# Performance work log

Measured on AMD Instinct MI355X. Metric: run time of the kernel, lower is better.

## Reference

```python
import jax, jax.numpy as jnp
import numpy as np

B, T, L, IN, D, H = 2, 16, 256, 768, 1024, 16
HD = D // H
NREG = 4
P = NREG + 2          # frozen prefix: registers + noise + action
DEPTH = 8
TINT = 4              # temporal_attention_interval
CTX = 30              # temporal_context_length
BASE = 1000.0         # rope_base
EPS = 1e-6            # qk_norm_eps / rmsnorm eps
HID = 4096            # 4.0 * latent_dim
S = L + P             # tokens per frame


def _rms(x, w=None, eps=EPS):
    y = x * jax.lax.rsqrt(jnp.mean(x * x, axis=-1, keepdims=True) + eps)
    return y * w if w is not None else y


def _rope_cache(n, hd, base):
    inv = base ** (-jnp.arange(0, hd, 2, dtype=jnp.float32) / hd)
    ang = jnp.arange(n, dtype=jnp.float32)[:, None] * inv[None, :]  # [n, hd/2]
    return jnp.cos(ang), jnp.sin(ang)


def _apply_rope(x, cos, sin):
    x1, x2 = x[..., ::2], x[..., 1::2]
    return jnp.stack([x1 * cos - x2 * sin, x1 * sin + x2 * cos], axis=-1).reshape(x.shape)


def _attn(x, Wqkv, Wo, cos, sin, mask):
    # x: [..., S, D]; mask: bool, True = attend, broadcastable to [..., H, S, S]
    qkv = x @ Wqkv
    q, k, v = jnp.split(qkv, 3, axis=-1)
    heads = lambda t: t.reshape(t.shape[:-1] + (H, HD)).swapaxes(-2, -3)  # [..., H, S, HD]
    q, k, v = heads(q), heads(k), heads(v)
    q = _apply_rope(_rms(q), cos, sin)   # qk-norm then RoPE
    k = _apply_rope(_rms(k), cos, sin)
    s = jnp.einsum('...qd,...kd->...qk', q, k) / jnp.sqrt(jnp.float32(HD))
    s = jnp.where(mask, s, jnp.float32(-1e9))
    p = jax.nn.softmax(s, axis=-1) * mask.any(axis=-1, keepdims=True)  # zero rows with no allowed keys
    o = jnp.einsum('...qk,...kd->...qd', p, v)
    return o.swapaxes(-2, -3).reshape(x.shape) @ Wo


def _spatial_mask():
    m = np.zeros((S, S), bool)
    r, n, a, ls = NREG, NREG, NREG + 1, NREG + 2
    m[ls:, ls:] = True; m[ls:, n] = True; m[ls:, a] = True; m[ls:, :r] = True
    m[n, n] = True; m[a, a] = True
    m[:r, ls:] = True; m[:r, n] = True; m[:r, a] = True; m[:r, :r] = True
    return jnp.asarray(m)


def _temporal_mask(indep):
    m = jnp.tril(jnp.ones((T, T), bool), -1)  # strictly-past causal
    if CTX is not None and CTX < T:
        m = m & jnp.triu(m, -CTX)             # sliding context window
    m = jnp.broadcast_to(m, (B, T, T))
    m = jnp.where(indep[:, None, None], False, m)
    return m[:, None, None]  # [B,1,1,T,T] -> broadcasts over token pos and heads


def setup_inputs() -> dict:
    key = jax.random.key(0)
    ks = iter(jax.random.split(key, 40))
    g = lambda shape, s=0.02: jax.random.normal(next(ks), shape, jnp.float32) * s
    inp = {
        'noisy_latents': jax.random.normal(next(ks), (B, T, L, IN), jnp.float32),
        'noise_levels': jax.random.uniform(next(ks), (B, T), jnp.float32),
        'actions': jax.random.normal(next(ks), (B, T, 6), jnp.float32),
        'independent_frames_mask': jnp.zeros((B,), bool),
        'actions_mask': jnp.ones((B, T), bool),
        'W_in': g((IN, D)),
        'noise_w1': g((1, D)), 'noise_b1': jnp.zeros((D,), jnp.float32),
        'noise_w2': g((D, D)), 'noise_b2': jnp.zeros((D,), jnp.float32),
        'base_action_embed': g((D,)),
        'action_w': g((6, D)), 'action_b': jnp.zeros((D,), jnp.float32),
        'registers': g((NREG, D)),
        'ln1_w': jnp.ones((DEPTH, D), jnp.float32),
        'Wqkv_s': g((DEPTH, D, 3 * D)), 'Wo_s': g((DEPTH, D, D)),
        'lnt_w': jnp.ones((DEPTH, D), jnp.float32),
        'Wqkv_t': g((DEPTH, D, 3 * D)), 'Wo_t': g((DEPTH, D, D)),
        'ln2_w': jnp.ones((DEPTH, D), jnp.float32),
        'W1': g((DEPTH, D, HID)), 'W2': g((DEPTH, D, HID)), 'W3': g((DEPTH, HID, D)),
        'final_w': jnp.ones((D,), jnp.float32),
        'W_out': g((D, IN)), 'b_out': jnp.zeros((IN,), jnp.float32),
    }
    return inp


def reference(noisy_latents, noise_levels, actions, independent_frames_mask, actions_mask,
              W_in, noise_w1, noise_b1, noise_w2, noise_b2, base_action_embed,
              action_w, action_b, registers, ln1_w, Wqkv_s, Wo_s, lnt_w, Wqkv_t, Wo_t,
              ln2_w, W1, W2, W3, final_w, W_out, b_out):
    noisy_tokens = noisy_latents @ W_in                                   # [B,T,L,D]
    base = jnp.broadcast_to(base_action_embed, (B, T, 1, D))
    act = base + (actions @ action_w + action_b)[:, :, None, :]
    act = jnp.where(actions_mask[:, :, None, None], act, base)            # [B,T,1,D]
    nz = jax.nn.silu(noise_levels[..., None] @ noise_w1 + noise_b1) @ noise_w2 + noise_b2
    nz = nz[:, :, None, :]                                                # [B,T,1,D]
    reg = jnp.broadcast_to(registers, (B, T, NREG, D))
    x = jnp.concatenate([reg, nz, act, noisy_tokens], axis=2)             # [B,T,S,D]

    sp_mask = _spatial_mask()
    tm_mask = _temporal_mask(independent_frames_mask)
    sp_cos, sp_sin = _rope_cache(S, HD, BASE)
    tm_cos, tm_sin = _rope_cache(T, HD, BASE)
    keep_tok = (jnp.arange(S) >= P)[None, :, None, None]                  # zero temporal update on frozen prefix

    for i in range(DEPTH):
        h = _rms(x, ln1_w[i])
        x = x + _attn(h, Wqkv_s[i], Wo_s[i], sp_cos, sp_sin, sp_mask)
        if i % TINT == 0:
            ht = _rms(x, lnt_w[i]).transpose(0, 2, 1, 3)                  # [B,S,T,D]
            ot = _attn(ht, Wqkv_t[i], Wo_t[i], tm_cos, tm_sin, tm_mask)
            x = x + (ot * keep_tok).transpose(0, 2, 1, 3)
        h2 = _rms(x, ln2_w[i])
        x = x + (jax.nn.silu(h2 @ W1[i]) * (h2 @ W2[i])) @ W3[i]

    latents = _rms(x[..., P:, :], final_w)
    pred_clean_latents = latents @ W_out + b_out                          # [B,T,L,IN]
    return pred_clean_latents
```

## Files before the change

kernel.cpp:

```cpp
#include <hip/hip_runtime.h>
#include <cstdint>
#include <cstddef>

#define DEV __device__ __forceinline__

typedef __attribute__((ext_vector_type(8))) __bf16 bf16x8;
typedef __attribute__((ext_vector_type(4))) float f32x4;

#define NTOK   8384
#define NTOKP  8448
#define NLAT   8192

DEV float b2f(unsigned short u) {
  unsigned int x = ((unsigned int)u) << 16;
  return __builtin_bit_cast(float, x);
}
DEV unsigned short f2b(float f) {
  unsigned int x = __builtin_bit_cast(unsigned int, f);
  x += 0x7fffu + ((x >> 16) & 1u);
  return (unsigned short)(x >> 16);
}
DEV float wred_sum(float v) {
#pragma unroll
  for (int o = 32; o; o >>= 1) v += __shfl_xor(v, o);
  return v;
}
DEV bool mask_or(const void* p, int i) {
  return ((const unsigned char*)p)[i] != 0 || ((const int*)p)[i] != 0;
}
DEV bool mask_and(const void* p, int i) {
  return ((const unsigned char*)p)[i] != 0 && ((const int*)p)[i] != 0;
}
DEV void wgb() {
  asm volatile("" ::: "memory");
  __builtin_amdgcn_s_barrier();
  asm volatile("" ::: "memory");
}


__global__ void conv_f2b(const float* __restrict__ in, unsigned short* __restrict__ out, int n4) {
  int i = blockIdx.x * 256 + threadIdx.x;
  if (i < n4) {
    float4 v = ((const float4*)in)[i];
    ushort4 o;
    o.x = f2b(v.x); o.y = f2b(v.y); o.z = f2b(v.z); o.w = f2b(v.w);
    ((ushort4*)out)[i] = o;
  }
}

__global__ void build_rope(float2* __restrict__ out, int npos) {
  int idx = blockIdx.x * 256 + threadIdx.x;
  if (idx >= npos * 32) return;
  int pos = idx >> 5, i = idx & 31;
  float inv = powf(1000.0f, -(float)(2 * i) * (1.0f / 64.0f));
  float ang = (float)pos * inv;
  float sv, cv;
  sincosf(ang, &sv, &cv);
  out[idx] = make_float2(cv, sv);
}

__global__ __launch_bounds__(256) void transpose_w(const float* __restrict__ in,
                                                   unsigned short* __restrict__ out,
                                                   int K, int N, int ostride) {
  __shared__ float tile[32][33];
  int kb = blockIdx.x * 32, nb = blockIdx.y * 32;
  int tx = threadIdx.x & 31, ty = threadIdx.x >> 5;
#pragma unroll
  for (int i = 0; i < 32; i += 8)
    tile[ty + i][tx] = in[(size_t)(kb + ty + i) * N + (nb + tx)];
  __syncthreads();
#pragma unroll
  for (int i = 0; i < 32; i += 8)
    out[(size_t)(nb + ty + i) * ostride + (kb + tx)] = f2b(tile[tx][ty + i]);
}

__global__ __launch_bounds__(256) void noise_h1(const float* __restrict__ nlvl,
                                                const float* __restrict__ w1,
                                                const float* __restrict__ b1,
                                                const float* __restrict__ b2,
                                                float* __restrict__ h1,
                                                float* __restrict__ nz) {
  int i = blockIdx.x * 256 + threadIdx.x;
  int bt = i >> 10, d = i & 1023;
  float v = nlvl[bt] * w1[d] + b1[d];
  h1[i] = v / (1.0f + expf(-v));
  nz[i] = b2[d];
}

__global__ __launch_bounds__(256) void noise_mm(const float* __restrict__ h1,
                                                const float* __restrict__ w2,
                                                float* __restrict__ nz) {
  __shared__ float hs[32][128];
  int kc = blockIdx.x >> 4, dpg = blockIdx.x & 15;
  int tid = threadIdx.x;
  int k0 = kc * 128;
  for (int idx = tid; idx < 32 * 128; idx += 256) {
    int bt = idx >> 7, k = idx & 127;
    hs[bt][k] = h1[bt * 1024 + k0 + k];
  }
  __syncthreads();
  int dp = dpg * 64 + (tid & 63);
  int bt0 = (tid >> 6) * 8;
  float acc[8] = {};
  for (int k = 0; k < 128; ++k) {
    float w = w2[(size_t)(k0 + k) * 1024 + dp];
#pragma unroll
    for (int j = 0; j < 8; ++j) acc[j] += hs[bt0 + j][k] * w;
  }
#pragma unroll
  for (int j = 0; j < 8; ++j) atomicAdd(&nz[(bt0 + j) * 1024 + dp], acc[j]);
}

__global__ void embed_special(float* __restrict__ x, const float* __restrict__ regs,
                              const float* __restrict__ nz, const float* __restrict__ base_emb,
                              const float* __restrict__ actions, const float* __restrict__ action_w,
                              const float* __restrict__ action_b,
                              const void* __restrict__ amask) {
  int bt = blockIdx.x, d = threadIdx.x;
  float* xr = x + (size_t)bt * 262 * 1024;
#pragma unroll
  for (int r = 0; r < 4; ++r) xr[r * 1024 + d] = regs[r * 1024 + d];
  xr[4 * 1024 + d] = nz[(size_t)bt * 1024 + d];
  float a = base_emb[d];
  if (mask_or(amask, bt)) {
    float s = action_b[d];
#pragma unroll
    for (int i = 0; i < 6; ++i) s += actions[bt * 6 + i] * action_w[i * 1024 + d];
    a += s;
  }
  xr[5 * 1024 + d] = a;
}

template <bool REMAP>
__global__ __launch_bounds__(256) void rms_k(const float* __restrict__ x,
                                             const float* __restrict__ w,
                                             unsigned short* __restrict__ out) {
  int m = blockIdx.x, tid = threadIdx.x;
  size_t src = REMAP ? ((size_t)(m >> 8) * 262 + 6 + (m & 255)) : (size_t)m;
  float4 v = ((const float4*)(x + src * 1024))[tid];
  float ss = v.x * v.x + v.y * v.y + v.z * v.z + v.w * v.w;
  ss = wred_sum(ss);
  __shared__ float sred[4];
  if ((tid & 63) == 0) sred[tid >> 6] = ss;
  __syncthreads();
  float tot = sred[0] + sred[1] + sred[2] + sred[3];
  float sc = rsqrtf(tot * (1.0f / 1024.0f) + 1e-6f);
  float4 wv = ((const float4*)w)[tid];
  ushort4 o;
  o.x = f2b(v.x * sc * wv.x); o.y = f2b(v.y * sc * wv.y);
  o.z = f2b(v.z * sc * wv.z); o.w = f2b(v.w * sc * wv.w);
  ((ushort4*)(out + (size_t)m * 1024))[tid] = o;
}

#define KSTR 72
#define VSTR 296
__global__ __launch_bounds__(256) void attn_spatial(const unsigned short* __restrict__ qkv,
                                                    unsigned short* __restrict__ o,
                                                    const float2* __restrict__ rope) {
  __shared__ unsigned short Ks[272 * KSTR];
  __shared__ unsigned short Vt[64 * VSTR];
  __shared__ unsigned short Ps[4][16 * VSTR];
  const int h = blockIdx.x & 15;
  const int bt = blockIdx.x >> 4;
  const int tid = threadIdx.x, wave = tid >> 6, lane = tid & 63;
  const size_t tb = (size_t)bt * 262;

  {
    const int d = lane;
#pragma unroll 1
    for (int pss = 0; pss < 17; ++pss) {
      const int t0 = (pss * 4 + wave) * 4;
      ushort4 vp;
      unsigned short* vpp = (unsigned short*)&vp;
#pragma unroll
      for (int j = 0; j < 4; ++j) {
        const int t = t0 + j;
        float kv = 0.f, vv = 0.f;
        if (t < 262) {
          const size_t rb = (tb + t) * 3072 + h * 64 + d;
          kv = b2f(qkv[rb + 1024]);
          vv = b2f(qkv[rb + 2048]);
        }
        float ss = wred_sum(kv * kv);
        kv *= rsqrtf(ss * (1.0f / 64.0f) + 1e-6f);
        float partner = __shfl_xor(kv, 1);
        const int tc = t < 262 ? t : 261;
        float2 cs = rope[tc * 32 + (d >> 1)];
        kv = ((d & 1) == 0) ? (kv * cs.x - partner * cs.y)
                            : (partner * cs.y + kv * cs.x);
        Ks[t * KSTR + d] = f2b(kv);
        vpp[j] = f2b(vv);
      }
      *(ushort4*)(&Vt[d * VSTR + t0]) = vp;
    }
    for (int idx = tid; idx < 64 * 24; idx += 256) {
      Vt[(idx / 24) * VSTR + 272 + (idx % 24)] = 0;
    }
    for (int idx = tid; idx < 4 * 16 * 34; idx += 256) {
      int w = idx / (16 * 34), r = (idx / 34) & 15, c = idx % 34;
      Ps[w][r * VSTR + 262 + c] = 0;
    }
  }
  __syncthreads();

  unsigned short* Pw = &Ps[wave][0];
  const int kcol = lane & 15;
  const int g8 = (lane >> 4) << 3;
  const int g4 = g8 >> 1;
  const int rq = (lane >> 4) << 2;

#pragma unroll 1
  for (int qc = wave; qc < 17; qc += 4) {
    const int q0 = qc * 16;
    const int qrow = q0 + kcol;
    const int grow = qrow < 262 ? qrow : 261;
    const unsigned short* qp = qkv + (tb + grow) * 3072 + h * 64 + g8;
    float qv[16];
    {
      ushort4 a = *(const ushort4*)qp, b = *(const ushort4*)(qp + 4);
      ushort4 c = *(const ushort4*)(qp + 32), e = *(const ushort4*)(qp + 36);
      qv[0] = b2f(a.x); qv[1] = b2f(a.y); qv[2] = b2f(a.z); qv[3] = b2f(a.w);
      qv[4] = b2f(b.x); qv[5] = b2f(b.y); qv[6] = b2f(b.z); qv[7] = b2f(b.w);
      qv[8] = b2f(c.x); qv[9] = b2f(c.y); qv[10] = b2f(c.z); qv[11] = b2f(c.w);
      qv[12] = b2f(e.x); qv[13] = b2f(e.y); qv[14] = b2f(e.z); qv[15] = b2f(e.w);
    }
    float ss = 0.f;
#pragma unroll
    for (int i = 0; i < 16; ++i) ss += qv[i] * qv[i];
    ss += __shfl_xor(ss, 16);
    ss += __shfl_xor(ss, 32);
    const float qsc = rsqrtf(ss * (1.0f / 64.0f) + 1e-6f);
    bf16x8 aq0, aq1;
    unsigned short* u0 = (unsigned short*)&aq0;
    unsigned short* u1 = (unsigned short*)&aq1;
#pragma unroll
    for (int i = 0; i < 4; ++i) {
      float2 cs0 = rope[grow * 32 + g4 + i];
      float a = qv[2 * i] * qsc, b = qv[2 * i + 1] * qsc;
      u0[2 * i] = f2b(a * cs0.x - b * cs0.y);
      u0[2 * i + 1] = f2b(a * cs0.y + b * cs0.x);
      float2 cs1 = rope[grow * 32 + 16 + g4 + i];
      float a1 = qv[8 + 2 * i] * qsc, b1 = qv[9 + 2 * i] * qsc;
      u1[2 * i] = f2b(a1 * cs1.x - b1 * cs1.y);
      u1[2 * i + 1] = f2b(a1 * cs1.y + b1 * cs1.x);
    }
    f32x4 sc[17];
#pragma unroll
    for (int kc = 0; kc < 17; ++kc) {
      const unsigned short* kb = &Ks[(kc * 16 + kcol) * KSTR + g8];
      f32x4 z = {};
      z = __builtin_amdgcn_mfma_f32_16x16x32_bf16(aq0, *(const bf16x8*)kb, z, 0, 0, 0);
      sc[kc] = __builtin_amdgcn_mfma_f32_16x16x32_bf16(aq1, *(const bf16x8*)(kb + 32), z, 0, 0, 0);
    }
#pragma unroll
    for (int kc = 0; kc < 17; ++kc) {
      const int k = kc * 16 + kcol;
#pragma unroll
      for (int j = 0; j < 4; ++j) {
        const int sq = q0 + rq + j;
        const bool valid = (k < 262) && ((sq != 4 && sq != 5) || (k == sq));
        sc[kc][j] = valid ? sc[kc][j] * 0.125f : -1e30f;
      }
    }
    float sm[4];
#pragma unroll
    for (int j = 0; j < 4; ++j) {
      float m = -1e30f;
#pragma unroll
      for (int kc = 0; kc < 17; ++kc) m = fmaxf(m, sc[kc][j]);
#pragma unroll
      for (int off = 1; off < 16; off <<= 1) m = fmaxf(m, __shfl_xor(m, off));
      float s = 0.f;
#pragma unroll
      for (int kc = 0; kc < 17; ++kc) {
        float e = expf(sc[kc][j] - m);
        sc[kc][j] = e;
        s += e;
      }
#pragma unroll
      for (int off = 1; off < 16; off <<= 1) s += __shfl_xor(s, off);
      sm[j] = 1.0f / s;
    }
#pragma unroll
    for (int kc = 0; kc < 17; ++kc) {
      const int k = kc * 16 + kcol;
#pragma unroll
      for (int j = 0; j < 4; ++j)
        Pw[(rq + j) * VSTR + k] = f2b(sc[kc][j] * sm[j]);
    }
    f32x4 oacc[4] = {};
#pragma unroll
    for (int tc = 0; tc < 9; ++tc) {
      const bf16x8 ap = *(const bf16x8*)(&Pw[kcol * VSTR + tc * 32 + g8]);
#pragma unroll
      for (int nt = 0; nt < 4; ++nt) {
        const bf16x8 bv = *(const bf16x8*)(&Vt[(nt * 16 + kcol) * VSTR + tc * 32 + g8]);
        oacc[nt] = __builtin_amdgcn_mfma_f32_16x16x32_bf16(ap, bv, oacc[nt], 0, 0, 0);
      }
    }
#pragma unroll
    for (int nt = 0; nt < 4; ++nt) {
#pragma unroll
      for (int j = 0; j < 4; ++j) {
        const int sq = q0 + rq + j;
        if (sq < 262)
          o[(tb + sq) * 1024 + h * 64 + nt * 16 + kcol] = f2b(oacc[nt][j]);
      }
    }
  }
}

__global__ __launch_bounds__(256) void attn_temporal(const unsigned short* __restrict__ qkv,
                                                     unsigned short* __restrict__ o,
                                                     const float2* __restrict__ rope,
                                                     const void* __restrict__ indep) {
  int gw = blockIdx.x * 4 + (threadIdx.x >> 6);
  int lane = threadIdx.x & 63;
  if (gw >= NTOK) return;
  int h = gw & 15;
  int s = (gw >> 4) % 262;
  int b = (gw >> 4) / 262;
  bool dead = (s < 6) || mask_and(indep, b);
  float q[16], kk[16], vv[16], out[16];
#pragma unroll
  for (int t = 0; t < 16; ++t) {
    out[t] = 0.f;
    if (!dead) {
      size_t off = ((size_t)((b * 16 + t) * 262 + s)) * 3072 + h * 64 + lane;
      q[t] = b2f(qkv[off]);
      kk[t] = b2f(qkv[off + 1024]);
      vv[t] = b2f(qkv[off + 2048]);
    }
  }
  if (!dead) {
#pragma unroll
    for (int t = 0; t < 16; ++t) {
      float sq_ = wred_sum(q[t] * q[t]);
      float qv = q[t] * rsqrtf(sq_ * (1.0f / 64.0f) + 1e-6f);
      float sk_ = wred_sum(kk[t] * kk[t]);
      float kv = kk[t] * rsqrtf(sk_ * (1.0f / 64.0f) + 1e-6f);
      float2 cs = rope[t * 32 + (lane >> 1)];
      float qp = __shfl_xor(qv, 1);
      float kp = __shfl_xor(kv, 1);
      q[t] = ((lane & 1) == 0) ? (qv * cs.x - qp * cs.y) : (qp * cs.y + qv * cs.x);
      kk[t] = ((lane & 1) == 0) ? (kv * cs.x - kp * cs.y) : (kp * cs.y + kv * cs.x);
    }
#pragma unroll
    for (int t = 1; t < 16; ++t) {
      float m = -1e30f, l = 0.f, acc = 0.f;
#pragma unroll
      for (int j = 0; j < t; ++j) {
        float pr = q[t] * kk[j];
#pragma unroll
        for (int o2 = 32; o2; o2 >>= 1) pr += __shfl_xor(pr, o2);
        pr *= 0.125f;
        float mn = fmaxf(m, pr);
        float cor = expf(m - mn);
        float e = expf(pr - mn);
        l = l * cor + e;
        acc = acc * cor + e * vv[j];
        m = mn;
      }
      out[t] = acc / l;
    }
  }
#pragma unroll
  for (int t = 0; t < 16; ++t) {
    size_t off = ((size_t)((b * 16 + t) * 262 + s)) * 1024 + h * 64 + lane;
    o[off] = f2b(out[t]);
  }
}

DEV void stage_tiles(const unsigned short* __restrict__ A, const unsigned short* __restrict__ Bw,
                     size_t arow0, size_t brow0, int K, int k0,
                     unsigned short* As, unsigned short* Bs, int wave, int lane) {
  const int srow = lane >> 2;
  const int scol = (lane & 3) * 8;
#pragma unroll
  for (int c = 0; c < 2; ++c) {
    const int chunk = wave * 2 + c;
    unsigned short* ga = const_cast<unsigned short*>(A + (arow0 + chunk * 16 + srow) * K + k0 + scol);
    unsigned short* gb = const_cast<unsigned short*>(Bw + (brow0 + chunk * 16 + srow) * K + k0 + scol);
    __builtin_amdgcn_global_load_lds((__attribute__((address_space(1))) void*)ga,
                                     (__attribute__((address_space(3))) void*)(As + chunk * 512),
                                     16, 0, 0);
    __builtin_amdgcn_global_load_lds((__attribute__((address_space(1))) void*)gb,
                                     (__attribute__((address_space(3))) void*)(Bs + chunk * 512),
                                     16, 0, 0);
  }
}

template <int EPI>
__global__ __launch_bounds__(256) void gemm_k(const unsigned short* __restrict__ A,
                                              const unsigned short* __restrict__ Bw,
                                              void* __restrict__ C,
                                              const float* __restrict__ aux,
                                              int Mvalid, int K, int ldc) {
  __shared__ unsigned short As[2][128 * 32];
  __shared__ unsigned short Bs[2][128 * 32];
  const int tid = threadIdx.x;
  const int wave = tid >> 6, lane = tid & 63;
  const int wm = wave >> 1, wn = wave & 1;
  const size_t arow0 = (size_t)blockIdx.x * 128;
  const size_t brow0 = (size_t)blockIdx.y * 128;

  f32x4 acc[4][4] = {};
  const int KT = K >> 5;

  stage_tiles(A, Bw, arow0, brow0, K, 0, As[0], Bs[0], wave, lane);
  __syncthreads();
  int buf = 0;
  for (int kt = 0; kt < KT; ++kt) {
    if (kt + 1 < KT)
      stage_tiles(A, Bw, arow0, brow0, K, (kt + 1) << 5, As[buf ^ 1], Bs[buf ^ 1], wave, lane);
    const int kk = (lane >> 4) * 8;
    const int rsel = lane & 15;
    bf16x8 af[4], bfr[4];
#pragma unroll
    for (int mt = 0; mt < 4; ++mt)
      af[mt] = *reinterpret_cast<const bf16x8*>(&As[buf][(wm * 64 + mt * 16 + rsel) * 32 + kk]);
#pragma unroll
    for (int nt = 0; nt < 4; ++nt)
      bfr[nt] = *reinterpret_cast<const bf16x8*>(&Bs[buf][(wn * 64 + nt * 16 + rsel) * 32 + kk]);
#pragma unroll
    for (int mt = 0; mt < 4; ++mt) {
#pragma unroll
      for (int nt = 0; nt < 4; ++nt)
        acc[mt][nt] = __builtin_amdgcn_mfma_f32_16x16x32_bf16(af[mt], bfr[nt], acc[mt][nt], 0, 0, 0);
    }
    __syncthreads();
    buf ^= 1;
  }

  const int row_base = blockIdx.x * 128 + wm * 64;
  const int col_base = blockIdx.y * 128 + wn * 64;
#pragma unroll
  for (int mt = 0; mt < 4; ++mt) {
#pragma unroll
    for (int nt = 0; nt < 4; ++nt) {
      const int col = col_base + nt * 16 + (lane & 15);
      const int r0 = row_base + mt * 16 + ((lane >> 4) << 2);
#pragma unroll
      for (int j = 0; j < 4; ++j) {
        const int row = r0 + j;
        float v = acc[mt][nt][j];
        if (EPI == 2) {
          float partner = __shfl_xor(v, 1);
          if (row < Mvalid && !(lane & 1)) {
            float sv = v / (1.0f + expf(-v));
            ((unsigned short*)C)[(size_t)row * ldc + (col >> 1)] = f2b(sv * partner);
          }
        } else if (row < Mvalid) {
          if (EPI == 0) {
            ((unsigned short*)C)[(size_t)row * ldc + col] = f2b(v);
          } else if (EPI == 1) {
            float* p = (float*)C + (size_t)row * ldc + col;
            *p += v;
          } else if (EPI == 3) {
            ((float*)C)[(size_t)row * ldc + col] = v + aux[col];
          } else if (EPI == 4) {
            ((float*)C)[(size_t)row * ldc + col] = v;
          } else if (EPI == 5) {
            int xr = (row >> 8) * 262 + 6 + (row & 255);
            ((float*)C)[(size_t)xr * ldc + col] = v;
          }
        }
      }
    }
  }
}

DEV void stage256(const unsigned short* __restrict__ G, size_t row0, int K, int kt,
                  unsigned short* lds, int wid, int lane) {
  const int r0 = lane >> 2;
  const int csrc = (lane & 3) ^ (r0 & 3);
#pragma unroll
  for (int l = 0; l < 2; ++l) {
    const int row = wid * 32 + l * 16 + r0;
    unsigned short* g = const_cast<unsigned short*>(G + (row0 + row) * (size_t)K + kt * 32 + csrc * 8);
    __builtin_amdgcn_global_load_lds((__attribute__((address_space(1))) void*)g,
                                     (__attribute__((address_space(3))) void*)(lds + (wid * 2 + l) * 512),
                                     16, 0, 0);
  }
}

template <int EPI>
__global__ __launch_bounds__(512) void gemm256_k(const unsigned short* __restrict__ A,
                                                 const unsigned short* __restrict__ Bw,
                                                 void* __restrict__ C,
                                                 int Mvalid, int K, int ldc, int nbx) {
  __shared__ unsigned short As[4][8192];
  __shared__ unsigned short Bs[4][8192];
  const int tid = threadIdx.x;
  const int wid = tid >> 6, lane = tid & 63;
  const int wm = wid >> 2, wn = wid & 3;
  const int nwg = gridDim.x;
  const int qq = nwg >> 3, rr = nwg & 7;
  const int xcd = blockIdx.x & 7, idx = blockIdx.x >> 3;
  const int wg = (xcd < rr ? xcd * (qq + 1) : rr * (qq + 1) + (xcd - rr) * qq) + idx;
  const int bx = wg % nbx, by = wg / nbx;
  const size_t arow0 = (size_t)bx * 256;
  const size_t brow0 = (size_t)by * 256;
  const int NT = K >> 5;

  const int rsel = lane & 15;
  const int physc = ((lane >> 4) ^ (lane & 3)) << 3;

  f32x4 acc[8][4] = {};

  stage256(A, arow0, K, 0, As[0], wid, lane);
  stage256(Bw, brow0, K, 0, Bs[0], wid, lane);
  stage256(A, arow0, K, 1, As[1], wid, lane);
  stage256(Bw, brow0, K, 1, Bs[1], wid, lane);
  stage256(A, arow0, K, 2, As[2], wid, lane);
  stage256(Bw, brow0, K, 2, Bs[2], wid, lane);
  asm volatile("s_waitcnt vmcnt(8)" ::: "memory");
  wgb();

#pragma unroll 1
  for (int kt = 0; kt < NT; ++kt) {
    unsigned short* as = As[kt & 3];
    unsigned short* bs = Bs[kt & 3];
    bf16x8 bfr[4], af[4];
#pragma unroll
    for (int nt = 0; nt < 4; ++nt)
      bfr[nt] = *(const bf16x8*)(bs + (wn * 64 + nt * 16 + rsel) * 32 + physc);
#pragma unroll
    for (int mt = 0; mt < 4; ++mt)
      af[mt] = *(const bf16x8*)(as + (wm * 128 + mt * 16 + rsel) * 32 + physc);
    if (kt + 3 < NT) stage256(A, arow0, K, kt + 3, As[(kt + 3) & 3], wid, lane);
    wgb();
    __builtin_amdgcn_s_setprio(1);
#pragma unroll
    for (int mt = 0; mt < 4; ++mt)
#pragma unroll
      for (int nt = 0; nt < 4; ++nt)
        acc[mt][nt] = __builtin_amdgcn_mfma_f32_16x16x32_bf16(af[mt], bfr[nt], acc[mt][nt], 0, 0, 0);
    __builtin_amdgcn_s_setprio(0);
    wgb();
#pragma unroll
    for (int mt = 0; mt < 4; ++mt)
      af[mt] = *(const bf16x8*)(as + (wm * 128 + (mt + 4) * 16 + rsel) * 32 + physc);
    if (kt + 3 < NT) stage256(Bw, brow0, K, kt + 3, Bs[(kt + 3) & 3], wid, lane);
    wgb();
    __builtin_amdgcn_s_setprio(1);
#pragma unroll
    for (int mt = 0; mt < 4; ++mt)
#pragma unroll
      for (int nt = 0; nt < 4; ++nt)
        acc[mt + 4][nt] = __builtin_amdgcn_mfma_f32_16x16x32_bf16(af[mt], bfr[nt], acc[mt + 4][nt], 0, 0, 0);
    __builtin_amdgcn_s_setprio(0);
    if (kt + 3 < NT) {
      asm volatile("s_waitcnt vmcnt(8)" ::: "memory");
    } else if (kt + 2 < NT) {
      asm volatile("s_waitcnt vmcnt(4)" ::: "memory");
    } else if (kt + 1 < NT) {
      asm volatile("s_waitcnt vmcnt(0)" ::: "memory");
    }
    wgb();
  }

  const int row_base = bx * 256 + wm * 128;
  const int col_base = by * 256 + wn * 64;
#pragma unroll
  for (int mt = 0; mt < 8; ++mt) {
#pragma unroll
    for (int nt = 0; nt < 4; ++nt) {
      const int col = col_base + nt * 16 + rsel;
      const int r0 = row_base + mt * 16 + ((lane >> 4) << 2);
#pragma unroll
      for (int j = 0; j < 4; ++j) {
        const int row = r0 + j;
        float v = acc[mt][nt][j];
        if (EPI == 2) {
          float partner = __shfl_xor(v, 1);
          if (row < Mvalid && !(lane & 1)) {
            float sv = v / (1.0f + expf(-v));
            ((unsigned short*)C)[(size_t)row * ldc + (col >> 1)] = f2b(sv * partner);
          }
        } else if (row < Mvalid) {
          if (EPI == 0) {
            ((unsigned short*)C)[(size_t)row * ldc + col] = f2b(v);
          }
        }
      }
    }
  }
}

extern "C" void kernel_launch(void* const* d_in, const int* in_sizes, int n_in,
                              void* d_out, int out_size, void* d_ws, size_t ws_size,
                              hipStream_t stream) {
  const float* noisy = (const float*)d_in[0];
  const float* nlvl = (const float*)d_in[1];
  const float* actions = (const float*)d_in[2];
  const void* indep = d_in[3];
  const void* amask = d_in[4];
  const float* W_in = (const float*)d_in[5];
  const float* noise_w1 = (const float*)d_in[6];
  const float* noise_b1 = (const float*)d_in[7];
  const float* noise_w2 = (const float*)d_in[8];
  const float* noise_b2 = (const float*)d_in[9];
  const float* base_emb = (const float*)d_in[10];
  const float* action_w = (const float*)d_in[11];
  const float* action_b = (const float*)d_in[12];
  const float* registers = (const float*)d_in[13];
  const float* ln1_w = (const float*)d_in[14];
  const float* Wqkv_s = (const float*)d_in[15];
  const float* Wo_s = (const float*)d_in[16];
  const float* lnt_w = (const float*)d_in[17];
  const float* Wqkv_t = (const float*)d_in[18];
  const float* Wo_t = (const float*)d_in[19];
  const float* ln2_w = (const float*)d_in[20];
  const float* W1 = (const float*)d_in[21];
  const float* W2 = (const float*)d_in[22];
  const float* W3 = (const float*)d_in[23];
  const float* final_w = (const float*)d_in[24];
  const float* W_out = (const float*)d_in[25];
  const float* b_out = (const float*)d_in[26];

  char* p = (char*)d_ws;
  auto alloc = [&](size_t bytes) {
    char* r = p;
    p += (bytes + 255) & ~(size_t)255;
    return r;
  };
  float* X = (float*)alloc((size_t)NTOKP * 1024 * 4);
  unsigned short* HB = (unsigned short*)alloc((size_t)NTOKP * 1024 * 2);
  unsigned short* AO = (unsigned short*)alloc((size_t)NTOKP * 1024 * 2);
  char* SCR = alloc((size_t)NTOKP * 4096 * 2);
  unsigned short* QKV = (unsigned short*)SCR;
  unsigned short* G = (unsigned short*)SCR;
  unsigned short* NLB = (unsigned short*)SCR;
  float* NZ = (float*)alloc(32 * 1024 * 4);
  float* H1 = (float*)alloc(32 * 1024 * 4);
  float2* RSP = (float2*)alloc(262 * 32 * 8);
  float2* RTM = (float2*)alloc(16 * 32 * 8);
  unsigned short* WINT = (unsigned short*)alloc((size_t)1024 * 768 * 2);
  unsigned short* WQKVS = (unsigned short*)alloc((size_t)8 * 3072 * 1024 * 2);
  unsigned short* WOS = (unsigned short*)alloc((size_t)8 * 1024 * 1024 * 2);
  unsigned short* WQKVT = (unsigned short*)alloc((size_t)8 * 3072 * 1024 * 2);
  unsigned short* WOT = (unsigned short*)alloc((size_t)8 * 1024 * 1024 * 2);
  unsigned short* W12T = (unsigned short*)alloc((size_t)8 * 8192 * 1024 * 2);
  unsigned short* W3T = (unsigned short*)alloc((size_t)8 * 1024 * 4096 * 2);
  unsigned short* WOUTT = (unsigned short*)alloc((size_t)768 * 1024 * 2);

  auto tr = [&](const float* in, unsigned short* out, int K, int N, int ostride) {
    dim3 g(K / 32, N / 32);
    transpose_w<<<g, 256, 0, stream>>>(in, out, K, N, ostride);
  };
  tr(W_in, WINT, 768, 1024, 768);
  for (int i = 0; i < 8; ++i) {
    tr(Wqkv_s + (size_t)i * 1024 * 3072, WQKVS + (size_t)i * 3072 * 1024, 1024, 3072, 1024);
    tr(Wo_s + (size_t)i * 1024 * 1024, WOS + (size_t)i * 1024 * 1024, 1024, 1024, 1024);
    tr(Wqkv_t + (size_t)i * 1024 * 3072, WQKVT + (size_t)i * 3072 * 1024, 1024, 3072, 1024);
    tr(Wo_t + (size_t)i * 1024 * 1024, WOT + (size_t)i * 1024 * 1024, 1024, 1024, 1024);
    tr(W1 + (size_t)i * 1024 * 4096, W12T + (size_t)i * 8192 * 1024, 1024, 4096, 2048);
    tr(W2 + (size_t)i * 1024 * 4096, W12T + (size_t)i * 8192 * 1024 + 1024, 1024, 4096, 2048);
    tr(W3 + (size_t)i * 4096 * 1024, W3T + (size_t)i * 1024 * 4096, 4096, 1024, 4096);
  }
  tr(W_out, WOUTT, 1024, 768, 1024);

  build_rope<<<33, 256, 0, stream>>>(RSP, 262);
  build_rope<<<2, 256, 0, stream>>>(RTM, 16);
  conv_f2b<<<6144, 256, 0, stream>>>(noisy, NLB, (NLAT * 768) / 4);
  noise_h1<<<128, 256, 0, stream>>>(nlvl, noise_w1, noise_b1, noise_b2, H1, NZ);
  noise_mm<<<128, 256, 0, stream>>>(H1, noise_w2, NZ);
  embed_special<<<32, 1024, 0, stream>>>(X, registers, NZ, base_emb, actions, action_w, action_b, amask);
  {
    dim3 g(64, 8);
    gemm_k<5><<<g, 256, 0, stream>>>(NLB, WINT, X, nullptr, NLAT, 768, 1024);
  }

  for (int i = 0; i < 8; ++i) {
    rms_k<false><<<NTOK, 256, 0, stream>>>(X, ln1_w + i * 1024, HB);
    gemm256_k<0><<<33 * 12, 512, 0, stream>>>(HB, WQKVS + (size_t)i * 3072 * 1024, QKV, NTOK, 1024, 3072, 33);
    attn_spatial<<<512, 256, 0, stream>>>(QKV, AO, RSP);
    {
      dim3 g(66, 8);
      gemm_k<1><<<g, 256, 0, stream>>>(AO, WOS + (size_t)i * 1024 * 1024, X, nullptr, NTOK, 1024, 1024);
    }
    if ((i & 3) == 0) {
      rms_k<false><<<NTOK, 256, 0, stream>>>(X, lnt_w + i * 1024, HB);
      gemm256_k<0><<<33 * 12, 512, 0, stream>>>(HB, WQKVT + (size_t)i * 3072 * 1024, QKV, NTOK, 1024, 3072, 33);
      attn_temporal<<<2096, 256, 0, stream>>>(QKV, AO, RTM, indep);
      {
        dim3 g(66, 8);
        gemm_k<1><<<g, 256, 0, stream>>>(AO, WOT + (size_t)i * 1024 * 1024, X, nullptr, NTOK, 1024, 1024);
      }
    }
    rms_k<false><<<NTOK, 256, 0, stream>>>(X, ln2_w + i * 1024, HB);
    gemm256_k<2><<<33 * 32, 512, 0, stream>>>(HB, W12T + (size_t)i * 8192 * 1024, G, NTOK, 1024, 4096, 33);
    {
      dim3 g(66, 8);
      gemm_k<1><<<g, 256, 0, stream>>>(G, W3T + (size_t)i * 1024 * 4096, X, nullptr, NTOK, 4096, 1024);
    }
  }

  rms_k<true><<<NLAT, 256, 0, stream>>>(X, final_w, HB);
  {
    dim3 g(64, 6);
    gemm_k<3><<<g, 256, 0, stream>>>(HB, WOUTT, d_out, b_out, NLAT, 1024, 768);
  }
}
```

Baseline: 6.922 ms.

## Rework 256-tile GEMM staging to triple buffer with new LDS swizzle

```diff
diff --git a/kernel.cpp b/kernel.cpp
--- a/kernel.cpp
+++ b/kernel.cpp
@@ -444,22 +444,12 @@
       for (int j = 0; j < 4; ++j) {
         const int row = r0 + j;
         float v = acc[mt][nt][j];
-        if (EPI == 2) {
-          float partner = __shfl_xor(v, 1);
-          if (row < Mvalid && !(lane & 1)) {
-            float sv = v / (1.0f + expf(-v));
-            ((unsigned short*)C)[(size_t)row * ldc + (col >> 1)] = f2b(sv * partner);
-          }
-        } else if (row < Mvalid) {
-          if (EPI == 0) {
-            ((unsigned short*)C)[(size_t)row * ldc + col] = f2b(v);
-          } else if (EPI == 1) {
+        if (row < Mvalid) {
+          if (EPI == 1) {
             float* p = (float*)C + (size_t)row * ldc + col;
             *p += v;
           } else if (EPI == 3) {
             ((float*)C)[(size_t)row * ldc + col] = v + aux[col];
-          } else if (EPI == 4) {
-            ((float*)C)[(size_t)row * ldc + col] = v;
           } else if (EPI == 5) {
             int xr = (row >> 8) * 262 + 6 + (row & 255);
             ((float*)C)[(size_t)xr * ldc + col] = v;
@@ -470,66 +460,68 @@
   }
 }
 
-DEV void stage256(const unsigned short* __restrict__ G, size_t row0, int K, int kt,
-                  unsigned short* lds, int wid, int lane) {
-  const int r0 = lane >> 2;
-  const int csrc = (lane & 3) ^ (r0 & 3);
-#pragma unroll
-  for (int l = 0; l < 2; ++l) {
-    const int row = wid * 32 + l * 16 + r0;
-    unsigned short* g = const_cast<unsigned short*>(G + (row0 + row) * (size_t)K + kt * 32 + csrc * 8);
+DEV void stage1op(const unsigned short* __restrict__ G, size_t row0, int K, int kt,
+                  unsigned short* slot, int tid) {
+#pragma unroll
+  for (int i = 0; i < 2; ++i) {
+    const int p = i * 8192 + (tid << 4);
+    const int lg = p ^ (((p >> 7) & 3) << 4);
+    const int grow = lg >> 6;
+    const int gcol = (lg & 63) >> 1;
+    unsigned short* g = const_cast<unsigned short*>(G + (row0 + grow) * (size_t)K + kt * 32 + gcol);
     __builtin_amdgcn_global_load_lds((__attribute__((address_space(1))) void*)g,
-                                     (__attribute__((address_space(3))) void*)(lds + (wid * 2 + l) * 512),
+                                     (__attribute__((address_space(3))) void*)(slot + i * 4096 + (tid >> 6) * 512),
                                      16, 0, 0);
   }
+}
+
+DEV bf16x8 ldsfrag(const unsigned short* slot, int row, int ks16) {
+  const int l = row * 64 + ks16;
+  const int ph = l ^ (((l >> 7) & 3) << 4);
+  return *(const bf16x8*)((const char*)slot + ph);
 }
 
 template <int EPI>
 __global__ __launch_bounds__(512) void gemm256_k(const unsigned short* __restrict__ A,
                                                  const unsigned short* __restrict__ Bw,
                                                  void* __restrict__ C,
-                                                 int Mvalid, int K, int ldc, int nbx) {
-  __shared__ unsigned short As[4][8192];
-  __shared__ unsigned short Bs[4][8192];
+                                                 int Mvalid, int K, int ldc) {
+  __shared__ unsigned short As[3][8192];
+  __shared__ unsigned short Bs[3][8192];
   const int tid = threadIdx.x;
-  const int wid = tid >> 6, lane = tid & 63;
+  const int lane = tid & 63, wid = tid >> 6;
   const int wm = wid >> 2, wn = wid & 3;
-  const int nwg = gridDim.x;
-  const int qq = nwg >> 3, rr = nwg & 7;
-  const int xcd = blockIdx.x & 7, idx = blockIdx.x >> 3;
-  const int wg = (xcd < rr ? xcd * (qq + 1) : rr * (qq + 1) + (xcd - rr) * qq) + idx;
-  const int bx = wg % nbx, by = wg / nbx;
-  const size_t arow0 = (size_t)bx * 256;
-  const size_t brow0 = (size_t)by * 256;
+  const size_t arow0 = (size_t)blockIdx.x * 256;
+  const size_t brow0 = (size_t)blockIdx.y * 256;
   const int NT = K >> 5;
-
   const int rsel = lane & 15;
-  const int physc = ((lane >> 4) ^ (lane & 3)) << 3;
+  const int ks16 = (lane >> 4) << 4;
 
   f32x4 acc[8][4] = {};
 
-  stage256(A, arow0, K, 0, As[0], wid, lane);
-  stage256(Bw, brow0, K, 0, Bs[0], wid, lane);
-  stage256(A, arow0, K, 1, As[1], wid, lane);
-  stage256(Bw, brow0, K, 1, Bs[1], wid, lane);
-  stage256(A, arow0, K, 2, As[2], wid, lane);
-  stage256(Bw, brow0, K, 2, Bs[2], wid, lane);
-  asm volatile("s_waitcnt vmcnt(8)" ::: "memory");
+  stage1op(A, arow0, K, 0, As[0], tid);
+  stage1op(Bw, brow0, K, 0, Bs[0], tid);
+  stage1op(A, arow0, K, 1, As[1], tid);
+  stage1op(Bw, brow0, K, 1, Bs[1], tid);
+  asm volatile("s_waitcnt vmcnt(4)" ::: "memory");
   wgb();
 
 #pragma unroll 1
   for (int kt = 0; kt < NT; ++kt) {
-    unsigned short* as = As[kt & 3];
-    unsigned short* bs = Bs[kt & 3];
+    unsigned short* as = As[kt % 3];
+    unsigned short* bs = Bs[kt % 3];
+    unsigned short* wa = As[(kt + 2) % 3];
+    unsigned short* wb = Bs[(kt + 2) % 3];
+    const bool pf = (kt + 2) < NT;
     bf16x8 bfr[4], af[4];
 #pragma unroll
-    for (int nt = 0; nt < 4; ++nt)
-      bfr[nt] = *(const bf16x8*)(bs + (wn * 64 + nt * 16 + rsel) * 32 + physc);
-#pragma unroll
-    for (int mt = 0; mt < 4; ++mt)
-      af[mt] = *(const bf16x8*)(as + (wm * 128 + mt * 16 + rsel) * 32 + physc);
-    if (kt + 3 < NT) stage256(A, arow0, K, kt + 3, As[(kt + 3) & 3], wid, lane);
+    for (int nt = 0; nt < 4; ++nt) bfr[nt] = ldsfrag(bs, wn * 64 + nt * 16 + rsel, ks16);
+#pragma unroll
+    for (int mt = 0; mt < 4; ++mt) af[mt] = ldsfrag(as, wm * 128 + mt * 16 + rsel, ks16);
+    if (pf) stage1op(A, arow0, K, kt + 2, wa, tid);
     wgb();
+    asm volatile("s_waitcnt lgkmcnt(0)" ::: "memory");
+    __builtin_amdgcn_sched_barrier(0);
     __builtin_amdgcn_s_setprio(1);
 #pragma unroll
     for (int mt = 0; mt < 4; ++mt)
@@ -539,10 +531,11 @@
     __builtin_amdgcn_s_setprio(0);
     wgb();
 #pragma unroll
-    for (int mt = 0; mt < 4; ++mt)
-      af[mt] = *(const bf16x8*)(as + (wm * 128 + (mt + 4) * 16 + rsel) * 32 + physc);
-    if (kt + 3 < NT) stage256(Bw, brow0, K, kt + 3, Bs[(kt + 3) & 3], wid, lane);
+    for (int mt = 0; mt < 4; ++mt) af[mt] = ldsfrag(as, wm * 128 + (mt + 4) * 16 + rsel, ks16);
+    if (pf) stage1op(Bw, brow0, K, kt + 2, wb, tid);
     wgb();
+    asm volatile("s_waitcnt lgkmcnt(0)" ::: "memory");
+    __builtin_amdgcn_sched_barrier(0);
     __builtin_amdgcn_s_setprio(1);
 #pragma unroll
     for (int mt = 0; mt < 4; ++mt)
@@ -550,18 +543,18 @@
       for (int nt = 0; nt < 4; ++nt)
         acc[mt + 4][nt] = __builtin_amdgcn_mfma_f32_16x16x32_bf16(af[mt], bfr[nt], acc[mt + 4][nt], 0, 0, 0);
     __builtin_amdgcn_s_setprio(0);
-    if (kt + 3 < NT) {
-      asm volatile("s_waitcnt vmcnt(8)" ::: "memory");
-    } else if (kt + 2 < NT) {
-      asm volatile("s_waitcnt vmcnt(4)" ::: "memory");
-    } else if (kt + 1 < NT) {
-      asm volatile("s_waitcnt vmcnt(0)" ::: "memory");
+    if (kt + 1 < NT) {
+      if (pf) {
+        asm volatile("s_waitcnt vmcnt(4)" ::: "memory");
+      } else {
+        asm volatile("s_waitcnt vmcnt(0)" ::: "memory");
+      }
     }
     wgb();
   }
 
-  const int row_base = bx * 256 + wm * 128;
-  const int col_base = by * 256 + wn * 64;
+  const int row_base = blockIdx.x * 256 + wm * 128;
+  const int col_base = blockIdx.y * 256 + wn * 64;
 #pragma unroll
   for (int mt = 0; mt < 8; ++mt) {
 #pragma unroll
@@ -674,7 +667,10 @@
 
   for (int i = 0; i < 8; ++i) {
     rms_k<false><<<NTOK, 256, 0, stream>>>(X, ln1_w + i * 1024, HB);
-    gemm256_k<0><<<33 * 12, 512, 0, stream>>>(HB, WQKVS + (size_t)i * 3072 * 1024, QKV, NTOK, 1024, 3072, 33);
+    {
+      dim3 g(33, 12);
+      gemm256_k<0><<<g, 512, 0, stream>>>(HB, WQKVS + (size_t)i * 3072 * 1024, QKV, NTOK, 1024, 3072);
+    }
     attn_spatial<<<512, 256, 0, stream>>>(QKV, AO, RSP);
     {
       dim3 g(66, 8);
@@ -682,7 +678,10 @@
     }
     if ((i & 3) == 0) {
       rms_k<false><<<NTOK, 256, 0, stream>>>(X, lnt_w + i * 1024, HB);
-      gemm256_k<0><<<33 * 12, 512, 0, stream>>>(HB, WQKVT + (size_t)i * 3072 * 1024, QKV, NTOK, 1024, 3072, 33);
+      {
+        dim3 g(33, 12);
+        gemm256_k<0><<<g, 512, 0, stream>>>(HB, WQKVT + (size_t)i * 3072 * 1024, QKV, NTOK, 1024, 3072);
+      }
       attn_temporal<<<2096, 256, 0, stream>>>(QKV, AO, RTM, indep);
       {
         dim3 g(66, 8);
@@ -690,7 +689,10 @@
       }
     }
     rms_k<false><<<NTOK, 256, 0, stream>>>(X, ln2_w + i * 1024, HB);
-    gemm256_k<2><<<33 * 32, 512, 0, stream>>>(HB, W12T + (size_t)i * 8192 * 1024, G, NTOK, 1024, 4096, 33);
+    {
+      dim3 g(33, 32);
+      gemm256_k<2><<<g, 512, 0, stream>>>(HB, W12T + (size_t)i * 8192 * 1024, G, NTOK, 1024, 4096);
+    }
     {
       dim3 g(66, 8);
       gemm_k<1><<<g, 256, 0, stream>>>(G, W3T + (size_t)i * 1024 * 4096, X, nullptr, NTOK, 4096, 1024);
```

Result: no change. 6.828 ms (-1.4%).
